# Performance work log

Measured on AMD Instinct MI355X. Metric: run time of the kernel, lower is better.

Reference implementation:

```python
import jax, jax.numpy as jnp
import numpy as np

NUM_PARTS = 10
COP_W = 10.0
COP_K = 100.0
RES = 0.7874


def setup_inputs() -> dict:
    key = jax.random.key(0)
    k1, k2, k3, k4, k5, k6 = jax.random.split(key, 6)
    B, V, F, NHD = 256, 6890, 13776, 20000
    vertices = jax.random.normal(k1, (B, V, 3), dtype=jnp.float32)
    pressure = jax.random.uniform(k2, (B, 120, 40), dtype=jnp.float32)
    bw = jax.random.uniform(k3, (NHD, 3), dtype=jnp.float32)
    bary_w = bw / bw.sum(axis=1, keepdims=True)  # barycentric weights sum to 1
    faces = jax.random.randint(k4, (F, 3), 0, V, dtype=jnp.int64)
    face_sample = jax.random.randint(k5, (NHD,), 0, F, dtype=jnp.int64)
    face_part = jax.random.randint(k6, (F,), 0, NUM_PARTS, dtype=jnp.int64)
    return {"vertices": vertices, "pressure": pressure, "bary_w": bary_w,
            "faces": faces, "face_sample": face_sample, "face_part": face_part}


def cal_cop(pressure, resolution=RES):
    B, Y, X = pressure.shape
    x_coords = jnp.arange(X, dtype=pressure.dtype)
    y_coords = jnp.arange(Y, dtype=pressure.dtype)
    total = pressure.sum(axis=(1, 2))
    total = jnp.where(total == 0, jnp.asarray(1e-8, pressure.dtype), total)
    x_ws = (pressure * x_coords).sum(axis=(1, 2))
    y_ws = (pressure * y_coords[:, None]).sum(axis=(1, 2))
    x_c = x_ws / total
    y_c = y_ws / total
    cop_x = 0.01 * (x_c - 18.0) / resolution
    cop_y = 0.01 * (86.0 - y_c) / resolution
    cop_xy = jnp.stack([cop_x, cop_y, jnp.zeros_like(cop_x)], axis=1)
    cop_sensor_xy = jnp.stack([x_c, y_c], axis=1)
    return cop_xy, cop_sensor_xy


def reference(vertices, pressure, bary_w, faces, face_sample, face_part):
    # ---- per-part volume: signed tetrahedron volume per face, segment-summed per part
    tri = vertices[:, faces]                       # [B, F, 3, 3]
    v0, v1, v2 = tri[:, :, 0], tri[:, :, 1], tri[:, :, 2]
    tet = jnp.einsum('bfi,bfi->bf', v0, jnp.cross(v1, v2)) / 6.0   # [B, F]
    per_part_volume = jax.vmap(
        lambda t: jax.ops.segment_sum(t, face_part, num_segments=NUM_PARTS)
    )(tet)                                          # [B, P]

    # ---- HD mesh: barycentric sampling of 20000 points from faces
    fv = faces[face_sample]                         # [NHD, 3]
    vertices_hd = jnp.einsum('bnkc,nk->bnc', vertices[:, fv], bary_w)  # [B, NHD, 3]

    # ---- vertex-id -> part-volume mapping (one-hot sparse matmul == gather)
    vol_per_vert = per_part_volume[:, face_part[face_sample]]          # [B, NHD]

    com = (vertices_hd * vol_per_vert[..., None]).sum(axis=1) / \
          vol_per_vert.sum(axis=1, keepdims=True)                      # [B, 3]
    com_xy = jnp.stack([com[:, 0], com[:, 1], jnp.zeros_like(com[:, 0])], axis=1)
    com_mat = jnp.stack([com[:, 0] * 48.0, (59.0 / 33.0 - com[:, 1]) * 33.0], axis=1)

    cop_xy, _cop_mat = cal_cop(pressure)

    eps = 1e-6
    vh = vertices_hd[:, :, 1]                       # height above ground plane
    inside = (vh < 0.0).astype(vh.dtype)
    pw = inside * (1.0 - COP_K * vh) + (1.0 - inside) * jnp.exp(-COP_W * vh)
    cop = (vertices_hd * pw[..., None]).sum(axis=1) / (pw.sum(axis=1, keepdims=True) + eps)
    cop_mat_ipman = jnp.stack([cop[:, 0] + 18.0 / 78.74,
                               86.0 / 78.74 - cop[:, 1]], axis=1) * 100.0 * 0.7874

    stability_loss = jnp.linalg.norm(com_xy - cop_xy, axis=1).mean()
    return stability_loss, com_mat, cop_mat_ipman
```

## Files before the change

kernel.cpp:

```cpp
#include <hip/hip_runtime.h>
#include <math.h>

#define NB 256
#define NV 6890
#define NF 13776
#define NHD 20000
#define NPARTS 10
#define PY 120
#define PX 40
#define THREADS 1024
#define NWAVES (THREADS / 64)

#define WS_DIST_OFF  0
#define WS_TABF_OFF  1024
#define WS_TABS_OFF  (WS_TABF_OFF + NF * 16)
#define WS_TABW_OFF  (WS_TABS_OFF + NHD * 16)
#define WS_NEEDED    (WS_TABW_OFF + NHD * 16)

__device__ __forceinline__ float wred(float v) {
#pragma unroll
    for (int off = 32; off; off >>= 1) v += __shfl_down(v, off, 64);
    return v;
}

__global__ __launch_bounds__(256) void build_tabs(const int* __restrict__ faces,
                                                  const int* __restrict__ face_part,
                                                  const int* __restrict__ face_sample,
                                                  const float* __restrict__ bary_w,
                                                  int4* __restrict__ tabF,
                                                  int4* __restrict__ tabS,
                                                  float4* __restrict__ tabW) {
    const int i = blockIdx.x * 256 + threadIdx.x;
    if (i < NF)
        tabF[i] = make_int4(faces[3 * i + 0], faces[3 * i + 1], faces[3 * i + 2], face_part[i]);
    if (i < NHD) {
        const int fs = face_sample[i];
        tabS[i] = make_int4(faces[3 * fs + 0], faces[3 * fs + 1], faces[3 * fs + 2], face_part[fs]);
        tabW[i] = make_float4(bary_w[3 * i + 0], bary_w[3 * i + 1], bary_w[3 * i + 2], 0.0f);
    }
}

__device__ __forceinline__ float tet_of(const float* __restrict__ svx,
                                        const float* __restrict__ svy,
                                        const float* __restrict__ svz, int4 q) {
    const float ax = svx[q.x], bx = svx[q.y], cx = svx[q.z];
    const float ay = svy[q.x], by = svy[q.y], cy = svy[q.z];
    const float az = svz[q.x], bz = svz[q.y], cz = svz[q.z];
    return (ax * (by * cz - bz * cy) + ay * (bz * cx - bx * cz) + az * (bx * cy - by * cx)) *
           (1.0f / 6.0f);
}

template <bool TAB>
__global__ __launch_bounds__(THREADS, 4) void stab_main(
    const float* __restrict__ vertices,
    const float* __restrict__ pressure,
    const float* __restrict__ bary_w,
    const int*   __restrict__ faces,
    const int*   __restrict__ face_sample,
    const int*   __restrict__ face_part,
    const int4*  __restrict__ tabF,
    const int4*  __restrict__ tabS,
    const float4* __restrict__ tabW,
    float* __restrict__ out,
    float* __restrict__ dist)
{
    const int b    = blockIdx.x;
    const int tid  = threadIdx.x;
    const int wave = tid >> 6;
    const int lane = tid & 63;

    __shared__ float svx[NV];
    __shared__ float svy[NV];
    __shared__ float svz[NV];
    __shared__ float red[NWAVES][12];
    __shared__ float ppv[NPARTS];

    const float* vb = vertices + (size_t)b * (NV * 3);
    for (int v = tid; v < NV; v += THREADS) {
        svx[v] = vb[3 * v + 0];
        svy[v] = vb[3 * v + 1];
        svz[v] = vb[3 * v + 2];
    }
    __syncthreads();

    float pv[NPARTS];
#pragma unroll
    for (int p = 0; p < NPARTS; ++p) pv[p] = 0.0f;

    if constexpr (TAB) {
        for (int f0 = tid; f0 < NF; f0 += 4 * THREADS) {
            const int f1 = f0 + THREADS, f2 = f0 + 2 * THREADS, f3 = f0 + 3 * THREADS;
            const int g1 = min(f1, NF - 1), g2 = min(f2, NF - 1), g3 = min(f3, NF - 1);
            const int4 q0 = tabF[f0];
            const int4 q1 = tabF[g1];
            const int4 q2 = tabF[g2];
            const int4 q3 = tabF[g3];
            const float m1 = (f1 < NF) ? 1.0f : 0.0f;
            const float m2 = (f2 < NF) ? 1.0f : 0.0f;
            const float m3 = (f3 < NF) ? 1.0f : 0.0f;
            const float t0 = tet_of(svx, svy, svz, q0);
            const float t1 = tet_of(svx, svy, svz, q1) * m1;
            const float t2 = tet_of(svx, svy, svz, q2) * m2;
            const float t3 = tet_of(svx, svy, svz, q3) * m3;
#pragma unroll
            for (int p = 0; p < NPARTS; ++p) {
                pv[p] += (q0.w == p) ? t0 : 0.0f;
                pv[p] += (q1.w == p) ? t1 : 0.0f;
                pv[p] += (q2.w == p) ? t2 : 0.0f;
                pv[p] += (q3.w == p) ? t3 : 0.0f;
            }
        }
    } else {
        for (int f = tid; f < NF; f += THREADS) {
            const int4 q = make_int4(faces[3 * f + 0], faces[3 * f + 1], faces[3 * f + 2],
                                     face_part[f]);
            const float t = tet_of(svx, svy, svz, q);
#pragma unroll
            for (int p = 0; p < NPARTS; ++p) pv[p] += (q.w == p) ? t : 0.0f;
        }
    }
#pragma unroll
    for (int p = 0; p < NPARTS; ++p) {
        const float r = wred(pv[p]);
        if (lane == 0) red[wave][p] = r;
    }
    __syncthreads();
    if (tid < NPARTS) {
        float s = 0.0f;
#pragma unroll
        for (int w = 0; w < NWAVES; ++w) s += red[w][tid];
        ppv[tid] = s;
    }
    __syncthreads();

    float cnx = 0.f, cny = 0.f, cd = 0.f;
    float pnx = 0.f, pny = 0.f, pd = 0.f;

    if constexpr (TAB) {
        for (int n0 = tid; n0 < NHD; n0 += 4 * THREADS) {
            const int n1 = n0 + THREADS, n2 = n0 + 2 * THREADS, n3 = n0 + 3 * THREADS;
            const int h1 = min(n1, NHD - 1), h2 = min(n2, NHD - 1), h3 = min(n3, NHD - 1);
            const int4 q0 = tabS[n0];
            const int4 q1 = tabS[h1];
            const int4 q2 = tabS[h2];
            const int4 q3 = tabS[h3];
            const float4 w0 = tabW[n0];
            const float4 w1 = tabW[h1];
            const float4 w2 = tabW[h2];
            const float4 w3 = tabW[h3];
            const float m1 = (n1 < NHD) ? 1.0f : 0.0f;
            const float m2 = (n2 < NHD) ? 1.0f : 0.0f;
            const float m3 = (n3 < NHD) ? 1.0f : 0.0f;

            const float hx0 = w0.x * svx[q0.x] + w0.y * svx[q0.y] + w0.z * svx[q0.z];
            const float hy0 = w0.x * svy[q0.x] + w0.y * svy[q0.y] + w0.z * svy[q0.z];
            const float hx1 = w1.x * svx[q1.x] + w1.y * svx[q1.y] + w1.z * svx[q1.z];
            const float hy1 = w1.x * svy[q1.x] + w1.y * svy[q1.y] + w1.z * svy[q1.z];
            const float hx2 = w2.x * svx[q2.x] + w2.y * svx[q2.y] + w2.z * svx[q2.z];
            const float hy2 = w2.x * svy[q2.x] + w2.y * svy[q2.y] + w2.z * svy[q2.z];
            const float hx3 = w3.x * svx[q3.x] + w3.y * svx[q3.y] + w3.z * svx[q3.z];
            const float hy3 = w3.x * svy[q3.x] + w3.y * svy[q3.y] + w3.z * svy[q3.z];

            const float vol0 = ppv[q0.w];
            const float vol1 = ppv[q1.w] * m1;
            const float vol2 = ppv[q2.w] * m2;
            const float vol3 = ppv[q3.w] * m3;

            const float pw0 = ((hy0 < 0.0f) ? (1.0f - 100.0f * hy0) : __expf(-10.0f * hy0));
            const float pw1 = ((hy1 < 0.0f) ? (1.0f - 100.0f * hy1) : __expf(-10.0f * hy1)) * m1;
            const float pw2 = ((hy2 < 0.0f) ? (1.0f - 100.0f * hy2) : __expf(-10.0f * hy2)) * m2;
            const float pw3 = ((hy3 < 0.0f) ? (1.0f - 100.0f * hy3) : __expf(-10.0f * hy3)) * m3;

            cnx += hx0 * vol0 + hx1 * vol1 + hx2 * vol2 + hx3 * vol3;
            cny += hy0 * vol0 + hy1 * vol1 + hy2 * vol2 + hy3 * vol3;
            cd  += vol0 + vol1 + vol2 + vol3;
            pnx += hx0 * pw0 + hx1 * pw1 + hx2 * pw2 + hx3 * pw3;
            pny += hy0 * pw0 + hy1 * pw1 + hy2 * pw2 + hy3 * pw3;
            pd  += pw0 + pw1 + pw2 + pw3;
        }
    } else {
        for (int n = tid; n < NHD; n += THREADS) {
            const int fs = face_sample[n];
            const int i0 = faces[3 * fs + 0], i1 = faces[3 * fs + 1], i2 = faces[3 * fs + 2];
            const float w0 = bary_w[3 * n + 0], w1 = bary_w[3 * n + 1], w2 = bary_w[3 * n + 2];
            const float hx = w0 * svx[i0] + w1 * svx[i1] + w2 * svx[i2];
            const float hy = w0 * svy[i0] + w1 * svy[i1] + w2 * svy[i2];
            const float vol = ppv[face_part[fs]];
            cnx += hx * vol; cny += hy * vol; cd += vol;
            const float pw = (hy < 0.0f) ? (1.0f - 100.0f * hy) : __expf(-10.0f * hy);
            pnx += hx * pw; pny += hy * pw; pd += pw;
        }
    }

    float pt = 0.f, pxs = 0.f, pys = 0.f;
    const float* pb = pressure + (size_t)b * (PY * PX);
    for (int i = tid; i < PY * PX; i += THREADS) {
        const float p  = pb[i];
        const float xi = (float)(i % PX);
        const float yi = (float)(i / PX);
        pt  += p;
        pxs += p * xi;
        pys += p * yi;
    }

    float vals[9] = {cnx, cny, cd, pnx, pny, pd, pt, pxs, pys};
#pragma unroll
    for (int k = 0; k < 9; ++k) {
        const float r = wred(vals[k]);
        if (lane == 0) red[wave][k] = r;
    }
    __syncthreads();

    if (tid == 0) {
        float s[9];
#pragma unroll
        for (int k = 0; k < 9; ++k) {
            float acc = 0.0f;
#pragma unroll
            for (int w = 0; w < NWAVES; ++w) acc += red[w][k];
            s[k] = acc;
        }
        const float comx  = s[0] / s[2];
        const float comy  = s[1] / s[2];
        const float copx  = s[3] / (s[5] + 1e-6f);
        const float copy_ = s[4] / (s[5] + 1e-6f);

        out[1 + 2 * b + 0] = comx * 48.0f;
        out[1 + 2 * b + 1] = (59.0f / 33.0f - comy) * 33.0f;
        out[1 + 2 * NB + 2 * b + 0] = (copx + 18.0f / 78.74f) * (100.0f * 0.7874f);
        out[1 + 2 * NB + 2 * b + 1] = (86.0f / 78.74f - copy_) * (100.0f * 0.7874f);

        const float total = (s[6] == 0.0f) ? 1e-8f : s[6];
        const float xc = s[7] / total;
        const float yc = s[8] / total;
        const float pcopx = 0.01f * (xc - 18.0f) / 0.7874f;
        const float pcopy = 0.01f * (86.0f - yc) / 0.7874f;

        const float dx = comx - pcopx;
        const float dy = comy - pcopy;
        dist[b] = sqrtf(dx * dx + dy * dy);
    }
}

__global__ __launch_bounds__(256) void stab_reduce(const float* __restrict__ dist,
                                                   float* __restrict__ out) {
    const int tid = threadIdx.x;
    float v = dist[tid];
    v = wred(v);
    __shared__ float red[4];
    if ((tid & 63) == 0) red[tid >> 6] = v;
    __syncthreads();
    if (tid == 0) out[0] = (red[0] + red[1] + red[2] + red[3]) * (1.0f / 256.0f);
}

extern "C" void kernel_launch(void* const* d_in, const int* in_sizes, int n_in,
                              void* d_out, int out_size, void* d_ws, size_t ws_size,
                              hipStream_t stream) {
    const float* vertices    = (const float*)d_in[0];
    const float* pressure    = (const float*)d_in[1];
    const float* bary_w      = (const float*)d_in[2];
    const int*   faces       = (const int*)d_in[3];
    const int*   face_sample = (const int*)d_in[4];
    const int*   face_part   = (const int*)d_in[5];
    float* out = (float*)d_out;
    char*  ws  = (char*)d_ws;

    float* dist = (float*)(ws + WS_DIST_OFF);

    if (ws_size >= (size_t)WS_NEEDED) {
        int4*   tabF = (int4*)(ws + WS_TABF_OFF);
        int4*   tabS = (int4*)(ws + WS_TABS_OFF);
        float4* tabW = (float4*)(ws + WS_TABW_OFF);
        build_tabs<<<(NHD + 255) / 256, 256, 0, stream>>>(faces, face_part, face_sample,
                                                          bary_w, tabF, tabS, tabW);
        stab_main<true><<<NB, THREADS, 0, stream>>>(vertices, pressure, bary_w, faces,
                                                    face_sample, face_part, tabF, tabS, tabW,
                                                    out, dist);
    } else {
        stab_main<false><<<NB, THREADS, 0, stream>>>(vertices, pressure, bary_w, faces,
                                                     face_sample, face_part, nullptr, nullptr,
                                                     nullptr, out, dist);
    }
    stab_reduce<<<1, 256, 0, stream>>>(dist, out);
}
```

Before: 37.23 us.

## Fuse final reduction via last-block atomic, pad HD tables, prefetch loads, vectorize pressure

Drops the separate final reduce launch. The last block to finish, detected with an atomic counter reset in build_tabs, now computes the mean. The HD sample tables are padded to a multiple of 4*THREADS with zero-weight entries, which removes the per-iteration bounds masks, and the next group of table entries is software-prefetched into registers before the current group is processed. The part-volume table is replicated 32 ways in shared memory to avoid bank conflicts on the gather, and the pressure moments are read as float4. It adds a threadfence and atomic per block plus extra register pressure.

```diff
diff --git a/kernel.cpp b/kernel.cpp
--- a/kernel.cpp
+++ b/kernel.cpp
@@ -5,6 +5,7 @@
 #define NV 6890
 #define NF 13776
 #define NHD 20000
+#define NHDP 20480
 #define NPARTS 10
 #define PY 120
 #define PX 40
@@ -12,10 +13,11 @@
 #define NWAVES (THREADS / 64)
 
 #define WS_DIST_OFF  0
-#define WS_TABF_OFF  1024
+#define WS_CTR_OFF   1024
+#define WS_TABF_OFF  2048
 #define WS_TABS_OFF  (WS_TABF_OFF + NF * 16)
-#define WS_TABW_OFF  (WS_TABS_OFF + NHD * 16)
-#define WS_NEEDED    (WS_TABW_OFF + NHD * 16)
+#define WS_TABW_OFF  (WS_TABS_OFF + NHDP * 16)
+#define WS_NEEDED    (WS_TABW_OFF + NHDP * 16)
 
 __device__ __forceinline__ float wred(float v) {
 #pragma unroll
@@ -29,14 +31,19 @@
                                                   const float* __restrict__ bary_w,
                                                   int4* __restrict__ tabF,
                                                   int4* __restrict__ tabS,
-                                                  float4* __restrict__ tabW) {
+                                                  float4* __restrict__ tabW,
+                                                  unsigned int* __restrict__ ctr) {
     const int i = blockIdx.x * 256 + threadIdx.x;
+    if (i == 0) *ctr = 0u;
     if (i < NF)
         tabF[i] = make_int4(faces[3 * i + 0], faces[3 * i + 1], faces[3 * i + 2], face_part[i]);
     if (i < NHD) {
         const int fs = face_sample[i];
         tabS[i] = make_int4(faces[3 * fs + 0], faces[3 * fs + 1], faces[3 * fs + 2], face_part[fs]);
-        tabW[i] = make_float4(bary_w[3 * i + 0], bary_w[3 * i + 1], bary_w[3 * i + 2], 0.0f);
+        tabW[i] = make_float4(bary_w[3 * i + 0], bary_w[3 * i + 1], bary_w[3 * i + 2], 1.0f);
+    } else if (i < NHDP) {
+        tabS[i] = make_int4(0, 0, 0, 0);
+        tabW[i] = make_float4(0.0f, 0.0f, 0.0f, 0.0f);
     }
 }
 
@@ -62,18 +69,21 @@
     const int4*  __restrict__ tabS,
     const float4* __restrict__ tabW,
     float* __restrict__ out,
-    float* __restrict__ dist)
+    float* __restrict__ dist,
+    unsigned int* __restrict__ ctr)
 {
     const int b    = blockIdx.x;
     const int tid  = threadIdx.x;
     const int wave = tid >> 6;
     const int lane = tid & 63;
+    const int ln32 = tid & 31;
 
     __shared__ float svx[NV];
     __shared__ float svy[NV];
     __shared__ float svz[NV];
     __shared__ float red[NWAVES][12];
-    __shared__ float ppv[NPARTS];
+    __shared__ float ppvR[NPARTS * 32];
+    __shared__ int   slast;
 
     const float* vb = vertices + (size_t)b * (NV * 3);
     for (int v = tid; v < NV; v += THREADS) {
@@ -125,59 +135,54 @@
         if (lane == 0) red[wave][p] = r;
     }
     __syncthreads();
-    if (tid < NPARTS) {
+    if (tid < NPARTS * 32) {
+        const int p = tid >> 5;
         float s = 0.0f;
 #pragma unroll
-        for (int w = 0; w < NWAVES; ++w) s += red[w][tid];
-        ppv[tid] = s;
+        for (int w = 0; w < NWAVES; ++w) s += red[w][p];
+        ppvR[tid] = s;
     }
     __syncthreads();
 
     float cnx = 0.f, cny = 0.f, cd = 0.f;
     float pnx = 0.f, pny = 0.f, pd = 0.f;
 
+#define PROC_B()                                                                     \
+    _Pragma("unroll")                                                                \
+    for (int u = 0; u < 4; ++u) {                                                    \
+        const int4 q = qc[u];                                                        \
+        const float4 w = wc[u];                                                      \
+        const float hx = w.x * svx[q.x] + w.y * svx[q.y] + w.z * svx[q.z];           \
+        const float hy = w.x * svy[q.x] + w.y * svy[q.y] + w.z * svy[q.z];           \
+        const float vol = ppvR[(q.w << 5) + ln32] * w.w;                             \
+        const float pw = ((hy < 0.0f) ? (1.0f - 100.0f * hy) : __expf(-10.0f * hy))  \
+                         * w.w;                                                      \
+        cnx += hx * vol; cny += hy * vol; cd += vol;                                 \
+        pnx += hx * pw;  pny += hy * pw;  pd += pw;                                  \
+    }
+
     if constexpr (TAB) {
-        for (int n0 = tid; n0 < NHD; n0 += 4 * THREADS) {
-            const int n1 = n0 + THREADS, n2 = n0 + 2 * THREADS, n3 = n0 + 3 * THREADS;
-            const int h1 = min(n1, NHD - 1), h2 = min(n2, NHD - 1), h3 = min(n3, NHD - 1);
-            const int4 q0 = tabS[n0];
-            const int4 q1 = tabS[h1];
-            const int4 q2 = tabS[h2];
-            const int4 q3 = tabS[h3];
-            const float4 w0 = tabW[n0];
-            const float4 w1 = tabW[h1];
-            const float4 w2 = tabW[h2];
-            const float4 w3 = tabW[h3];
-            const float m1 = (n1 < NHD) ? 1.0f : 0.0f;
-            const float m2 = (n2 < NHD) ? 1.0f : 0.0f;
-            const float m3 = (n3 < NHD) ? 1.0f : 0.0f;
-
-            const float hx0 = w0.x * svx[q0.x] + w0.y * svx[q0.y] + w0.z * svx[q0.z];
-            const float hy0 = w0.x * svy[q0.x] + w0.y * svy[q0.y] + w0.z * svy[q0.z];
-            const float hx1 = w1.x * svx[q1.x] + w1.y * svx[q1.y] + w1.z * svx[q1.z];
-            const float hy1 = w1.x * svy[q1.x] + w1.y * svy[q1.y] + w1.z * svy[q1.z];
-            const float hx2 = w2.x * svx[q2.x] + w2.y * svx[q2.y] + w2.z * svx[q2.z];
-            const float hy2 = w2.x * svy[q2.x] + w2.y * svy[q2.y] + w2.z * svy[q2.z];
-            const float hx3 = w3.x * svx[q3.x] + w3.y * svx[q3.y] + w3.z * svx[q3.z];
-            const float hy3 = w3.x * svy[q3.x] + w3.y * svy[q3.y] + w3.z * svy[q3.z];
-
-            const float vol0 = ppv[q0.w];
-            const float vol1 = ppv[q1.w] * m1;
-            const float vol2 = ppv[q2.w] * m2;
-            const float vol3 = ppv[q3.w] * m3;
-
-            const float pw0 = ((hy0 < 0.0f) ? (1.0f - 100.0f * hy0) : __expf(-10.0f * hy0));
-            const float pw1 = ((hy1 < 0.0f) ? (1.0f - 100.0f * hy1) : __expf(-10.0f * hy1)) * m1;
-            const float pw2 = ((hy2 < 0.0f) ? (1.0f - 100.0f * hy2) : __expf(-10.0f * hy2)) * m2;
-            const float pw3 = ((hy3 < 0.0f) ? (1.0f - 100.0f * hy3) : __expf(-10.0f * hy3)) * m3;
-
-            cnx += hx0 * vol0 + hx1 * vol1 + hx2 * vol2 + hx3 * vol3;
-            cny += hy0 * vol0 + hy1 * vol1 + hy2 * vol2 + hy3 * vol3;
-            cd  += vol0 + vol1 + vol2 + vol3;
-            pnx += hx0 * pw0 + hx1 * pw1 + hx2 * pw2 + hx3 * pw3;
-            pny += hy0 * pw0 + hy1 * pw1 + hy2 * pw2 + hy3 * pw3;
-            pd  += pw0 + pw1 + pw2 + pw3;
-        }
+        int4   qc[4];
+        float4 wc[4];
+#pragma unroll
+        for (int u = 0; u < 4; ++u) {
+            qc[u] = tabS[tid + u * THREADS];
+            wc[u] = tabW[tid + u * THREADS];
+        }
+        for (int g = 0; g < 4; ++g) {
+            int4   qn[4];
+            float4 wn[4];
+            const int base = tid + 4 * (g + 1) * THREADS;
+#pragma unroll
+            for (int u = 0; u < 4; ++u) {
+                qn[u] = tabS[base + u * THREADS];
+                wn[u] = tabW[base + u * THREADS];
+            }
+            PROC_B();
+#pragma unroll
+            for (int u = 0; u < 4; ++u) { qc[u] = qn[u]; wc[u] = wn[u]; }
+        }
+        PROC_B();
     } else {
         for (int n = tid; n < NHD; n += THREADS) {
             const int fs = face_sample[n];
@@ -185,22 +190,25 @@
             const float w0 = bary_w[3 * n + 0], w1 = bary_w[3 * n + 1], w2 = bary_w[3 * n + 2];
             const float hx = w0 * svx[i0] + w1 * svx[i1] + w2 * svx[i2];
             const float hy = w0 * svy[i0] + w1 * svy[i1] + w2 * svy[i2];
-            const float vol = ppv[face_part[fs]];
+            const float vol = ppvR[(face_part[fs] << 5) + ln32];
             cnx += hx * vol; cny += hy * vol; cd += vol;
             const float pw = (hy < 0.0f) ? (1.0f - 100.0f * hy) : __expf(-10.0f * hy);
             pnx += hx * pw; pny += hy * pw; pd += pw;
         }
     }
+#undef PROC_B
 
     float pt = 0.f, pxs = 0.f, pys = 0.f;
-    const float* pb = pressure + (size_t)b * (PY * PX);
-    for (int i = tid; i < PY * PX; i += THREADS) {
-        const float p  = pb[i];
-        const float xi = (float)(i % PX);
-        const float yi = (float)(i / PX);
-        pt  += p;
-        pxs += p * xi;
-        pys += p * yi;
+    const float4* pb4 = (const float4*)(pressure + (size_t)b * (PY * PX));
+    for (int i = tid; i < (PY * PX) / 4; i += THREADS) {
+        const float4 v = pb4[i];
+        const int idx = 4 * i;
+        const float xb = (float)(idx % PX);
+        const float yb = (float)(idx / PX);
+        const float srow = v.x + v.y + v.z + v.w;
+        pt  += srow;
+        pxs += v.x * xb + v.y * (xb + 1.0f) + v.z * (xb + 2.0f) + v.w * (xb + 3.0f);
+        pys += srow * yb;
     }
 
     float vals[9] = {cnx, cny, cd, pnx, pny, pd, pt, pxs, pys};
@@ -239,6 +247,31 @@
         const float dx = comx - pcopx;
         const float dy = comy - pcopy;
         dist[b] = sqrtf(dx * dx + dy * dy);
+    }
+
+    if constexpr (TAB) {
+        if (tid == 0) {
+            __threadfence();
+            const unsigned int prev = atomicAdd(ctr, 1u);
+            slast = (prev == NB - 1) ? 1 : 0;
+        }
+        __syncthreads();
+        if (slast) {
+            __threadfence();
+            float v = 0.0f;
+            if (tid < NB)
+                v = __hip_atomic_load(&dist[tid], __ATOMIC_RELAXED,
+                                      __HIP_MEMORY_SCOPE_AGENT);
+            v = wred(v);
+            if (lane == 0) red[wave][0] = v;
+            __syncthreads();
+            if (tid == 0) {
+                float s = 0.0f;
+#pragma unroll
+                for (int w = 0; w < 4; ++w) s += red[w][0];
+                out[0] = s * (1.0f / NB);
+            }
+        }
     }
 }
 
@@ -265,21 +298,22 @@
     float* out = (float*)d_out;
     char*  ws  = (char*)d_ws;
 
-    float* dist = (float*)(ws + WS_DIST_OFF);
+    float* dist        = (float*)(ws + WS_DIST_OFF);
+    unsigned int* ctr  = (unsigned int*)(ws + WS_CTR_OFF);
 
     if (ws_size >= (size_t)WS_NEEDED) {
         int4*   tabF = (int4*)(ws + WS_TABF_OFF);
         int4*   tabS = (int4*)(ws + WS_TABS_OFF);
         float4* tabW = (float4*)(ws + WS_TABW_OFF);
-        build_tabs<<<(NHD + 255) / 256, 256, 0, stream>>>(faces, face_part, face_sample,
-                                                          bary_w, tabF, tabS, tabW);
+        build_tabs<<<(NHDP + 255) / 256, 256, 0, stream>>>(faces, face_part, face_sample,
+                                                           bary_w, tabF, tabS, tabW, ctr);
         stab_main<true><<<NB, THREADS, 0, stream>>>(vertices, pressure, bary_w, faces,
                                                     face_sample, face_part, tabF, tabS, tabW,
-                                                    out, dist);
+                                                    out, dist, ctr);
     } else {
         stab_main<false><<<NB, THREADS, 0, stream>>>(vertices, pressure, bary_w, faces,
                                                      face_sample, face_part, nullptr, nullptr,
-                                                     nullptr, out, dist);
-    }
-    stab_reduce<<<1, 256, 0, stream>>>(dist, out);
-}
+                                                     nullptr, out, dist, ctr);
+        stab_reduce<<<1, 256, 0, stream>>>(dist, out);
+    }
+}
```

After: 111.9 us. 201% more time.
